# Kernel optimization log

Measured on AMD Instinct MI355X. Metric: run time of the kernel, lower is better.

## Reference

```python
import jax, jax.numpy as jnp
import numpy as np

TOP_K = 2


def setup_inputs() -> dict:
    key = jax.random.key(0)
    k1, k2, k3, k4 = jax.random.split(key, 4)
    B, S, D, F, E = 4, 2048, 1024, 4096, 8
    return {
        "inputs": jax.random.normal(k1, (B, S, D), dtype=jnp.float32),
        "gate_w": jax.random.normal(k2, (D, E), dtype=jnp.float32) * 0.02,
        "w1": jax.random.normal(k3, (E, D, F), dtype=jnp.float32) * 0.02,
        "w2": jax.random.normal(k4, (E, F, D), dtype=jnp.float32) * 0.02,
    }


def reference(inputs, gate_w, w1, w2):
    # gate logits: [B, S, E]
    gate_logits = jnp.einsum("bsd,de->bse", inputs, gate_w)
    E = gate_logits.shape[-1]

    # router KL loss (matches F.kl_div(log(mean_prob), uniform, reduction='batchmean')):
    # kl = sum(u * (log u - log p_mean)) / E   (batchmean divides by first dim = E)
    gate_prob = jax.nn.softmax(gate_logits.astype(jnp.float32), axis=-1).astype(inputs.dtype)
    mean_prob = gate_prob.mean(axis=(0, 1))  # [E]
    u = jnp.full((E,), 1.0 / E, dtype=mean_prob.dtype)
    kl_loss = jnp.sum(u * (jnp.log(u) - jnp.log(mean_prob))) / E

    # top-k routing
    weights, selected = jax.lax.top_k(gate_logits, TOP_K)  # [B,S,k]
    prob = jax.nn.softmax(weights.astype(jnp.float32), axis=-1).astype(inputs.dtype)

    # combine weight per expert: [B,S,E]; zero for unselected experts
    onehot = jax.nn.one_hot(selected, E, dtype=prob.dtype)  # [B,S,k,E]
    combine = jnp.einsum("bsk,bske->bse", prob, onehot)

    results = jnp.zeros_like(inputs)
    for i in range(E):  # fixed small loop over experts
        h = jax.nn.silu(jnp.einsum("bsd,df->bsf", inputs, w1[i]))
        out = jnp.einsum("bsf,fd->bsd", h, w2[i])
        results = results + combine[..., i : i + 1] * out
    return (results, kl_loss)
```

## Files before the change

### kernel.cpp

```cpp
#include <hip/hip_runtime.h>
#include <hip/hip_bf16.h>
#include <cstdint>


#define N_TOK 8192
#define D_DIM 1024
#define F_DIM 4096
#define N_EXP 8
#define MB_MAX 136

#define CNT_OFF   0u
#define HOFF_OFF  64u
#define NMB_OFF   104u
#define ZPG_OFF   128u
#define MBE_OFF   256u
#define MBB_OFF   896u
#define PSUM_OFF  1536u
#define LIST_OFF  67072u
#define COEF_OFF  329216u
#define H1_OFF    1048576ull
#define XBF_OFF   1048576ull
#define W1T_OFF   18874368ull
#define W2T_OFF   (W1T_OFF + 67108864ull)
#define H2_OFF    (W2T_OFF + 67108864ull)
#define FULL_WS   (H2_OFF + 17408ull * 4096ull * 2ull)

typedef __attribute__((ext_vector_type(8))) short short8;
typedef __attribute__((ext_vector_type(4))) float f32x4;
typedef __attribute__((ext_vector_type(4))) float float4v;
typedef __attribute__((ext_vector_type(2))) unsigned int u32x2;

__device__ __forceinline__ unsigned short f2bf(float x) {
  unsigned int u = __float_as_uint(x);
  unsigned int r = (u + 0x7fffu + ((u >> 16) & 1u)) >> 16;
  return (unsigned short)r;
}

__device__ __forceinline__ void gload16(const void* g, void* l) {
  __builtin_amdgcn_global_load_lds(
      (const __attribute__((address_space(1))) void*)g,
      (__attribute__((address_space(3))) void*)l, 16, 0, 0);
}

__global__ void router_kernel(const float* __restrict__ x,
                              const float* __restrict__ gw,
                              int* __restrict__ cnt, int* __restrict__ list,
                              float* __restrict__ coef,
                              float* __restrict__ psum,
                              unsigned short* __restrict__ xbf) {
  const int wave = threadIdx.x >> 6;
  const int lane = threadIdx.x & 63;
  const int t = blockIdx.x * 4 + wave;

  __shared__ float bps[N_EXP];
  if (threadIdx.x < N_EXP) bps[threadIdx.x] = 0.f;
  __syncthreads();

  float lg[8] = {0.f, 0.f, 0.f, 0.f, 0.f, 0.f, 0.f, 0.f};
  const float* xr = x + (size_t)t * D_DIM;
  unsigned short* xbr = xbf + (size_t)t * D_DIM;
#pragma unroll
  for (int i = 0; i < 16; ++i) {
    int d = lane + i * 64;
    float xv = xr[d];
    xbr[d] = f2bf(xv);
    float4v w0 = *(const float4v*)(gw + d * 8);
    float4v w1 = *(const float4v*)(gw + d * 8 + 4);
    lg[0] = fmaf(xv, w0.x, lg[0]); lg[1] = fmaf(xv, w0.y, lg[1]);
    lg[2] = fmaf(xv, w0.z, lg[2]); lg[3] = fmaf(xv, w0.w, lg[3]);
    lg[4] = fmaf(xv, w1.x, lg[4]); lg[5] = fmaf(xv, w1.y, lg[5]);
    lg[6] = fmaf(xv, w1.z, lg[6]); lg[7] = fmaf(xv, w1.w, lg[7]);
  }
#pragma unroll
  for (int m = 32; m; m >>= 1) {
#pragma unroll
    for (int e = 0; e < 8; ++e) lg[e] += __shfl_xor(lg[e], m);
  }

  if (lane == 0) {
    float mx = lg[0];
#pragma unroll
    for (int e = 1; e < 8; ++e) mx = fmaxf(mx, lg[e]);
    float p[8], s = 0.f;
#pragma unroll
    for (int e = 0; e < 8; ++e) { p[e] = expf(lg[e] - mx); s += p[e]; }
    float inv = 1.f / s;
#pragma unroll
    for (int e = 0; e < 8; ++e) atomicAdd(&bps[e], p[e] * inv);

    int i0 = 0;
#pragma unroll
    for (int e = 1; e < 8; ++e) if (lg[e] > lg[i0]) i0 = e;
    int i1 = (i0 == 0) ? 1 : 0;
#pragma unroll
    for (int e = 0; e < 8; ++e) if (e != i1 && e != i0 && lg[e] > lg[i1]) i1 = e;
    float p0 = 1.f / (1.f + expf(lg[i1] - lg[i0]));
    float p1 = 1.f - p0;
    int s0 = atomicAdd(&cnt[i0], 1);
    list[i0 * N_TOK + s0] = t; coef[i0 * N_TOK + s0] = p0;
    int s1 = atomicAdd(&cnt[i1], 1);
    list[i1 * N_TOK + s1] = t; coef[i1 * N_TOK + s1] = p1;
  }
  __syncthreads();
  if (threadIdx.x < 8) psum[blockIdx.x * 8 + threadIdx.x] = bps[threadIdx.x];
}

__global__ void prefix_kernel(const int* __restrict__ cnt, int* __restrict__ hoff,
                              int* __restrict__ mbe, int* __restrict__ mbb,
                              int* __restrict__ nmb, int g) {
  if (threadIdx.x == 0) {
    int o = 0, gmb = 0;
    for (int e = 0; e < 8; ++e) {
      hoff[e] = o;
      int nb = (cnt[e] + g - 1) / g;
      for (int m = 0; m < nb; ++m) { mbe[gmb] = e; mbb[gmb] = m; ++gmb; }
      o += nb * g;
    }
    hoff[8] = o;
    *nmb = gmb;
  }
}

__global__ void kl_kernel(const float* __restrict__ psum, float* __restrict__ out_kl) {
  __shared__ float s[8];
  if (threadIdx.x < 8) s[threadIdx.x] = 0.f;
  __syncthreads();
  float loc[8] = {0.f, 0.f, 0.f, 0.f, 0.f, 0.f, 0.f, 0.f};
  for (int r = threadIdx.x; r < 2048; r += 256) {
#pragma unroll
    for (int e = 0; e < 8; ++e) loc[e] += psum[r * 8 + e];
  }
#pragma unroll
  for (int e = 0; e < 8; ++e) atomicAdd(&s[e], loc[e]);
  __syncthreads();
  if (threadIdx.x == 0) {
    float kl = 0.f;
#pragma unroll
    for (int e = 0; e < 8; ++e) {
      float mean = s[e] / 8192.f;
      kl += (logf(0.125f) - logf(mean));
    }
    out_kl[0] = kl * (0.125f * 0.125f);
  }
}

__global__ __launch_bounds__(256) void wtrans_kernel(
    const float* __restrict__ w, unsigned short* __restrict__ wt, int K, int N) {
  const int e = blockIdx.z;
  const int n0 = blockIdx.x * 64, k0 = blockIdx.y * 64;
  __shared__ float t[64][65];
  const float* we = w + (size_t)e * K * N;
  const int nl = threadIdx.x & 63;
  const int kl4 = threadIdx.x >> 6;
#pragma unroll
  for (int r = 0; r < 16; ++r) {
    int kl = r * 4 + kl4;
    t[kl][nl] = we[(size_t)(k0 + kl) * N + n0 + nl];
  }
  __syncthreads();
  unsigned short* wte = wt + (size_t)e * K * N;
  const int kp = (threadIdx.x & 31) * 2;
  const int nl8 = threadIdx.x >> 5;
#pragma unroll
  for (int r = 0; r < 8; ++r) {
    int n = r * 8 + nl8;
    unsigned int pk = (unsigned int)f2bf(t[kp][n]) |
                      ((unsigned int)f2bf(t[kp + 1][n]) << 16);
    *(unsigned int*)(wte + (size_t)(n0 + n) * K + k0 + kp) = pk;
  }
}

__device__ __forceinline__ short8 ld_frag(const unsigned short* base, int row_base,
                                          int k_base, int lane) {
  int row = row_base + (lane & 15);
  int byte = (row * 128 + (k_base + ((lane >> 4) << 3)) * 2) ^ ((row & 7) << 4);
  return *(const short8*)((const char*)base + byte);
}

#define STAGE4(buf)                                                        \
  {                                                                        \
    char* la_ = (char*)As + (buf) * 16384 + wave * 1024;                   \
    char* lb_ = (char*)Bs + (buf) * 16384 + wave * 1024;                   \
    _Pragma("unroll") for (int i_ = 0; i_ < 4; ++i_) {                     \
      gload16(asrc[i_], la_ + i_ * 4096);                                  \
      gload16(bsrc[i_], lb_ + i_ * 4096);                                  \
      asrc[i_] += astep[i_];                                               \
      bsrc[i_] += 128;                                                     \
    }                                                                      \
  }

__global__ __launch_bounds__(256, 2) void gemm1_v4(
    const unsigned short* __restrict__ xbf, const unsigned short* __restrict__ w1t,
    const int* __restrict__ cnt, const int* __restrict__ hoff,
    const int* __restrict__ mbe, const int* __restrict__ mbb,
    const int* __restrict__ nmb,
    const int* __restrict__ list, const unsigned short* __restrict__ zpage,
    unsigned short* __restrict__ h) {
  const int mb = blockIdx.y;
  if (mb >= *nmb) return;
  const int e = mbe[mb], mblk = mbb[mb], nblk = blockIdx.x;
  const int c = cnt[e];
  const int tid = threadIdx.x, lane = tid & 63, wave = tid >> 6;
  const int wm = (wave >> 1) * 64, wn = (wave & 1) * 64;

  __shared__ unsigned short As[2][8192];
  __shared__ unsigned short Bs[2][8192];

  const int rowb = tid >> 3;
  const int sw = (((tid & 7) ^ (rowb & 7)) << 4);
  const char* asrc[4]; int astep[4];
  const char* bsrc[4];
#pragma unroll
  for (int i = 0; i < 4; ++i) {
    int row = i * 32 + rowb;
    int slot = mblk * 128 + row;
    if (slot < c) {
      int tok = list[e * N_TOK + slot];
      asrc[i] = (const char*)(xbf + (size_t)tok * D_DIM) + sw;
      astep[i] = 128;
    } else {
      asrc[i] = (const char*)zpage + sw;
      astep[i] = 0;
    }
    bsrc[i] = (const char*)(w1t + ((size_t)e * F_DIM + nblk * 128 + row) * D_DIM) + sw;
  }

  f32x4 acc[4][4];
#pragma unroll
  for (int i = 0; i < 4; ++i)
#pragma unroll
    for (int j = 0; j < 4; ++j) acc[i][j] = f32x4{0.f, 0.f, 0.f, 0.f};

  STAGE4(0);
  __syncthreads();
  int cur = 0;
  for (int kc = 0; kc < 16; ++kc) {
    if (kc + 1 < 16) STAGE4(cur ^ 1);
    const unsigned short* At = As[cur];
    const unsigned short* Bt = Bs[cur];
#pragma unroll
    for (int ks = 0; ks < 2; ++ks) {
      short8 af[4], bb[4];
#pragma unroll
      for (int mf = 0; mf < 4; ++mf) af[mf] = ld_frag(At, wm + mf * 16, ks * 32, lane);
#pragma unroll
      for (int nf = 0; nf < 4; ++nf) bb[nf] = ld_frag(Bt, wn + nf * 16, ks * 32, lane);
#pragma unroll
      for (int mf = 0; mf < 4; ++mf)
#pragma unroll
        for (int nf = 0; nf < 4; ++nf)
          acc[mf][nf] = __builtin_amdgcn_mfma_f32_16x16x32_bf16(
              af[mf], bb[nf], acc[mf][nf], 0, 0, 0);
    }
    __syncthreads();
    cur ^= 1;
  }

  const int hbase = hoff[e] + mblk * 128;
#pragma unroll
  for (int mf = 0; mf < 4; ++mf)
#pragma unroll
    for (int nf = 0; nf < 4; ++nf)
#pragma unroll
      for (int r = 0; r < 4; ++r) {
        float v = acc[mf][nf][r];
        v = v / (1.f + __expf(-v));
        int row = wm + mf * 16 + ((lane >> 4) << 2) + r;
        int col = nblk * 128 + wn + nf * 16 + (lane & 15);
        h[(size_t)(hbase + row) * F_DIM + col] = f2bf(v);
      }
}

__global__ __launch_bounds__(256, 2) void gemm2_v4(
    const unsigned short* __restrict__ h, const unsigned short* __restrict__ w2t,
    const int* __restrict__ cnt, const int* __restrict__ hoff,
    const int* __restrict__ mbe, const int* __restrict__ mbb,
    const int* __restrict__ nmb,
    const int* __restrict__ list, const float* __restrict__ coef,
    float* __restrict__ out) {
  const int mb = blockIdx.y;
  if (mb >= *nmb) return;
  const int e = mbe[mb], mblk = mbb[mb], nblk = blockIdx.x;
  const int c = cnt[e];
  const int tid = threadIdx.x, lane = tid & 63, wave = tid >> 6;
  const int wm = (wave >> 1) * 64, wn = (wave & 1) * 64;

  __shared__ unsigned short As[2][8192];
  __shared__ unsigned short Bs[2][8192];

  const int rowb = tid >> 3;
  const int sw = (((tid & 7) ^ (rowb & 7)) << 4);
  const int hbase = hoff[e] + mblk * 128;
  const char* asrc[4]; int astep[4];
  const char* bsrc[4];
#pragma unroll
  for (int i = 0; i < 4; ++i) {
    int row = i * 32 + rowb;
    asrc[i] = (const char*)(h + (size_t)(hbase + row) * F_DIM) + sw;
    astep[i] = 128;
    bsrc[i] = (const char*)(w2t + ((size_t)e * D_DIM + nblk * 128 + row) * F_DIM) + sw;
  }

  f32x4 acc[4][4];
#pragma unroll
  for (int i = 0; i < 4; ++i)
#pragma unroll
    for (int j = 0; j < 4; ++j) acc[i][j] = f32x4{0.f, 0.f, 0.f, 0.f};

  STAGE4(0);
  __syncthreads();
  int cur = 0;
  for (int kc = 0; kc < 64; ++kc) {
    if (kc + 1 < 64) STAGE4(cur ^ 1);
    const unsigned short* At = As[cur];
    const unsigned short* Bt = Bs[cur];
#pragma unroll
    for (int ks = 0; ks < 2; ++ks) {
      short8 af[4], bb[4];
#pragma unroll
      for (int mf = 0; mf < 4; ++mf) af[mf] = ld_frag(At, wm + mf * 16, ks * 32, lane);
#pragma unroll
      for (int nf = 0; nf < 4; ++nf) bb[nf] = ld_frag(Bt, wn + nf * 16, ks * 32, lane);
#pragma unroll
      for (int mf = 0; mf < 4; ++mf)
#pragma unroll
        for (int nf = 0; nf < 4; ++nf)
          acc[mf][nf] = __builtin_amdgcn_mfma_f32_16x16x32_bf16(
              af[mf], bb[nf], acc[mf][nf], 0, 0, 0);
    }
    __syncthreads();
    cur ^= 1;
  }

#pragma unroll
  for (int mf = 0; mf < 4; ++mf) {
#pragma unroll
    for (int r = 0; r < 4; ++r) {
      int slot = mblk * 128 + wm + mf * 16 + ((lane >> 4) << 2) + r;
      if (slot < c) {
        int tok = list[e * N_TOK + slot];
        float cf = coef[e * N_TOK + slot];
#pragma unroll
        for (int nf = 0; nf < 4; ++nf) {
          int col = nblk * 128 + wn + nf * 16 + (lane & 15);
          unsafeAtomicAdd(&out[(size_t)tok * D_DIM + col], cf * acc[mf][nf][r]);
        }
      }
    }
  }
}

__global__ __launch_bounds__(256) void gemm1_v1(
    const float* __restrict__ x, const float* __restrict__ w1,
    const int* __restrict__ cnt, const int* __restrict__ hoff,
    const int* __restrict__ list, unsigned short* __restrict__ h) {
  const int e = blockIdx.z, mblk = blockIdx.y, nblk = blockIdx.x;
  const int c = cnt[e];
  if (mblk * 128 >= c) return;
  const int tid = threadIdx.x, lane = tid & 63, wave = tid >> 6;
  const int wm = (wave >> 1) * 64, wn = (wave & 1) * 64;

  __shared__ unsigned short At[128 * 64];
  __shared__ unsigned short Bt[128 * 64];
  __shared__ int toks[128];
  if (tid < 128) {
    int slot = mblk * 128 + tid;
    toks[tid] = (slot < c) ? list[e * N_TOK + slot] : -1;
  }
  __syncthreads();

  f32x4 acc[4][4];
#pragma unroll
  for (int i = 0; i < 4; ++i)
#pragma unroll
    for (int j = 0; j < 4; ++j) acc[i][j] = f32x4{0.f, 0.f, 0.f, 0.f};

  const float* w1e = w1 + (size_t)e * D_DIM * F_DIM;
  for (int kc = 0; kc < 16; ++kc) {
    __syncthreads();
#pragma unroll
    for (int it = 0; it < 8; ++it) {
      int lin = it * 256 + tid;
      int row = lin >> 4, c4 = lin & 15;
      int tok = toks[row];
      unsigned int lo = 0u, hi = 0u;
      if (tok >= 0) {
        float4v f = *(const float4v*)(x + (size_t)tok * D_DIM + kc * 64 + c4 * 4);
        lo = (unsigned int)f2bf(f.x) | ((unsigned int)f2bf(f.y) << 16);
        hi = (unsigned int)f2bf(f.z) | ((unsigned int)f2bf(f.w) << 16);
      }
      int byte = (row * 128 + c4 * 8) ^ ((row & 7) << 4);
      *(u32x2*)((char*)At + byte) = u32x2{lo, hi};
    }
#pragma unroll
    for (int it = 0; it < 16; ++it) {
      int lin = it * 256 + tid;
      int f_loc = lin & 127, dp = lin >> 7;
      int d = kc * 64 + dp * 2;
      const float* src = w1e + (size_t)d * F_DIM + nblk * 128 + f_loc;
      unsigned int pk = (unsigned int)f2bf(src[0]) |
                        ((unsigned int)f2bf(src[F_DIM]) << 16);
      int byte = (f_loc * 128 + dp * 4) ^ ((f_loc & 7) << 4);
      *(unsigned int*)((char*)Bt + byte) = pk;
    }
    __syncthreads();
#pragma unroll
    for (int ks = 0; ks < 2; ++ks) {
      short8 af[4], bb[4];
#pragma unroll
      for (int mf = 0; mf < 4; ++mf) af[mf] = ld_frag(At, wm + mf * 16, ks * 32, lane);
#pragma unroll
      for (int nf = 0; nf < 4; ++nf) bb[nf] = ld_frag(Bt, wn + nf * 16, ks * 32, lane);
#pragma unroll
      for (int mf = 0; mf < 4; ++mf)
#pragma unroll
        for (int nf = 0; nf < 4; ++nf)
          acc[mf][nf] = __builtin_amdgcn_mfma_f32_16x16x32_bf16(
              af[mf], bb[nf], acc[mf][nf], 0, 0, 0);
    }
  }

  const int hbase = hoff[e] + mblk * 128;
#pragma unroll
  for (int mf = 0; mf < 4; ++mf)
#pragma unroll
    for (int nf = 0; nf < 4; ++nf)
#pragma unroll
      for (int r = 0; r < 4; ++r) {
        float v = acc[mf][nf][r];
        v = v / (1.f + __expf(-v));
        int row = wm + mf * 16 + ((lane >> 4) << 2) + r;
        int col = nblk * 128 + wn + nf * 16 + (lane & 15);
        h[(size_t)(hbase + row) * F_DIM + col] = f2bf(v);
      }
}

__global__ __launch_bounds__(256) void gemm2_v1(
    const unsigned short* __restrict__ h, const float* __restrict__ w2,
    const int* __restrict__ cnt, const int* __restrict__ hoff,
    const int* __restrict__ list, const float* __restrict__ coef,
    float* __restrict__ out) {
  const int e = blockIdx.z, mblk = blockIdx.y, nblk = blockIdx.x;
  const int c = cnt[e];
  if (mblk * 128 >= c) return;
  const int tid = threadIdx.x, lane = tid & 63, wave = tid >> 6;
  const int wm = (wave >> 1) * 64, wn = (wave & 1) * 64;

  __shared__ unsigned short At[128 * 64];
  __shared__ unsigned short Bt[128 * 64];

  f32x4 acc[4][4];
#pragma unroll
  for (int i = 0; i < 4; ++i)
#pragma unroll
    for (int j = 0; j < 4; ++j) acc[i][j] = f32x4{0.f, 0.f, 0.f, 0.f};

  const int hbase = hoff[e] + mblk * 128;
  const float* w2e = w2 + (size_t)e * F_DIM * D_DIM;
  for (int kc = 0; kc < 64; ++kc) {
    __syncthreads();
#pragma unroll
    for (int it = 0; it < 8; ++it) {
      int lin = it * 256 + tid;
      int row = lin >> 4, c4 = lin & 15;
      u32x2 v = *(const u32x2*)(h + (size_t)(hbase + row) * F_DIM + kc * 64 + c4 * 4);
      int byte = (row * 128 + c4 * 8) ^ ((row & 7) << 4);
      *(u32x2*)((char*)At + byte) = v;
    }
#pragma unroll
    for (int it = 0; it < 16; ++it) {
      int lin = it * 256 + tid;
      int dcol = lin & 127, kp = lin >> 7;
      int k = kc * 64 + kp * 2;
      const float* src = w2e + (size_t)k * D_DIM + nblk * 128 + dcol;
      unsigned int pk = (unsigned int)f2bf(src[0]) |
                        ((unsigned int)f2bf(src[D_DIM]) << 16);
      int byte = (dcol * 128 + kp * 4) ^ ((dcol & 7) << 4);
      *(unsigned int*)((char*)Bt + byte) = pk;
    }
    __syncthreads();
#pragma unroll
    for (int ks = 0; ks < 2; ++ks) {
      short8 af[4], bb[4];
#pragma unroll
      for (int mf = 0; mf < 4; ++mf) af[mf] = ld_frag(At, wm + mf * 16, ks * 32, lane);
#pragma unroll
      for (int nf = 0; nf < 4; ++nf) bb[nf] = ld_frag(Bt, wn + nf * 16, ks * 32, lane);
#pragma unroll
      for (int mf = 0; mf < 4; ++mf)
#pragma unroll
        for (int nf = 0; nf < 4; ++nf)
          acc[mf][nf] = __builtin_amdgcn_mfma_f32_16x16x32_bf16(
              af[mf], bb[nf], acc[mf][nf], 0, 0, 0);
    }
  }

#pragma unroll
  for (int mf = 0; mf < 4; ++mf) {
#pragma unroll
    for (int r = 0; r < 4; ++r) {
      int slot = mblk * 128 + wm + mf * 16 + ((lane >> 4) << 2) + r;
      if (slot < c) {
        int tok = list[e * N_TOK + slot];
        float cf = coef[e * N_TOK + slot];
#pragma unroll
        for (int nf = 0; nf < 4; ++nf) {
          int col = nblk * 128 + wn + nf * 16 + (lane & 15);
          unsafeAtomicAdd(&out[(size_t)tok * D_DIM + col], cf * acc[mf][nf][r]);
        }
      }
    }
  }
}

extern "C" void kernel_launch(void* const* d_in, const int* in_sizes, int n_in,
                              void* d_out, int out_size, void* d_ws, size_t ws_size,
                              hipStream_t stream) {
  const float* x = (const float*)d_in[0];
  const float* gw = (const float*)d_in[1];
  const float* w1 = (const float*)d_in[2];
  const float* w2 = (const float*)d_in[3];
  float* out = (float*)d_out;
  char* ws = (char*)d_ws;

  int* cnt = (int*)(ws + CNT_OFF);
  int* hoff = (int*)(ws + HOFF_OFF);
  int* nmb = (int*)(ws + NMB_OFF);
  int* mbe = (int*)(ws + MBE_OFF);
  int* mbb = (int*)(ws + MBB_OFF);
  float* psum = (float*)(ws + PSUM_OFF);
  int* list = (int*)(ws + LIST_OFF);
  float* coef = (float*)(ws + COEF_OFF);
  unsigned short* xbf = (unsigned short*)(ws + XBF_OFF);

  hipMemsetAsync(d_ws, 0, PSUM_OFF + 2048 * 8 * 4, stream);
  hipMemsetAsync(d_out, 0, (size_t)out_size * 4, stream);

  router_kernel<<<2048, 256, 0, stream>>>(x, gw, cnt, list, coef, psum, xbf);
  prefix_kernel<<<1, 64, 0, stream>>>(cnt, hoff, mbe, mbb, nmb, 128);
  kl_kernel<<<1, 256, 0, stream>>>(psum, out + 8388608);

  if (ws_size >= FULL_WS) {
    unsigned short* w1t = (unsigned short*)(ws + W1T_OFF);
    unsigned short* w2t = (unsigned short*)(ws + W2T_OFF);
    unsigned short* h = (unsigned short*)(ws + H2_OFF);
    const unsigned short* zpage = (const unsigned short*)(ws + ZPG_OFF);

    wtrans_kernel<<<dim3(64, 16, 8), 256, 0, stream>>>(w1, w1t, 1024, 4096);
    wtrans_kernel<<<dim3(16, 64, 8), 256, 0, stream>>>(w2, w2t, 4096, 1024);
    gemm1_v4<<<dim3(32, MB_MAX), 256, 0, stream>>>(xbf, w1t, cnt, hoff, mbe, mbb,
                                                   nmb, list, zpage, h);
    gemm2_v4<<<dim3(8, MB_MAX), 256, 0, stream>>>(h, w2t, cnt, hoff, mbe, mbb,
                                                  nmb, list, coef, out);
  } else {
    unsigned short* h = (unsigned short*)(ws + H1_OFF);
    gemm1_v1<<<dim3(32, 64, 8), 256, 0, stream>>>(x, w1, cnt, hoff, list, h);
    gemm2_v1<<<dim3(8, 64, 8), 256, 0, stream>>>(h, w2, cnt, hoff, list, coef, out);
  }
}
```

Baseline: 956.7 us.

## Enlarge grouped GEMM tiles to 256x256 with 8 waves and split-K gemm2

Both expert GEMMs move from 128x128 tiles with 4 waves to 256x256 tiles with 8 waves, each wave holding a 128x64 accumulator. This raises arithmetic intensity and cuts redundant global loads of the weights and activations. The K loop now uses explicit vmcnt waits, fenced barriers and s_setprio around the MFMA bursts to overlap loads with compute. gemm2 also splits K across two z-blocks that combine through the existing atomic adds. The costs are heavier register and LDS pressure, more padding waste per expert at the 256-row granularity, and extra atomic traffic.

```diff
diff --git a/kernel.cpp b/kernel.cpp
--- a/kernel.cpp
+++ b/kernel.cpp
@@ -7,7 +7,7 @@
 #define D_DIM 1024
 #define F_DIM 4096
 #define N_EXP 8
-#define MB_MAX 136
+#define MB_MAX 72
 
 #define CNT_OFF   0u
 #define HOFF_OFF  64u
@@ -23,7 +23,7 @@
 #define W1T_OFF   18874368ull
 #define W2T_OFF   (W1T_OFF + 67108864ull)
 #define H2_OFF    (W2T_OFF + 67108864ull)
-#define FULL_WS   (H2_OFF + 17408ull * 4096ull * 2ull)
+#define FULL_WS   (H2_OFF + 18432ull * 4096ull * 2ull)
 
 typedef __attribute__((ext_vector_type(8))) short short8;
 typedef __attribute__((ext_vector_type(4))) float f32x4;
@@ -177,19 +177,56 @@
   return *(const short8*)((const char*)base + byte);
 }
 
-#define STAGE4(buf)                                                        \
+#define ISSUE(b)                                                           \
   {                                                                        \
-    char* la_ = (char*)As + (buf) * 16384 + wave * 1024;                   \
-    char* lb_ = (char*)Bs + (buf) * 16384 + wave * 1024;                   \
+    char* la_ = (char*)&As[b][0] + tid * 16;                               \
+    char* lb_ = (char*)&Bs[b][0] + tid * 16;                               \
     _Pragma("unroll") for (int i_ = 0; i_ < 4; ++i_) {                     \
-      gload16(asrc[i_], la_ + i_ * 4096);                                  \
-      gload16(bsrc[i_], lb_ + i_ * 4096);                                  \
+      gload16(asrc[i_], la_ + i_ * 8192);                                  \
+      gload16(bsrc[i_], lb_ + i_ * 8192);                                  \
       asrc[i_] += astep[i_];                                               \
       bsrc[i_] += 128;                                                     \
     }                                                                      \
   }
 
-__global__ __launch_bounds__(256, 2) void gemm1_v4(
+#define COMPUTE(b)                                                         \
+  _Pragma("unroll") for (int ks_ = 0; ks_ < 2; ++ks_) {                    \
+    short8 af[8], bb[4];                                                   \
+    _Pragma("unroll") for (int mf_ = 0; mf_ < 8; ++mf_)                    \
+      af[mf_] = ld_frag(&As[b][0], wm + mf_ * 16, ks_ * 32, lane);         \
+    _Pragma("unroll") for (int nf_ = 0; nf_ < 4; ++nf_)                    \
+      bb[nf_] = ld_frag(&Bs[b][0], wn + nf_ * 16, ks_ * 32, lane);         \
+    __builtin_amdgcn_s_setprio(1);                                         \
+    _Pragma("unroll") for (int mf_ = 0; mf_ < 8; ++mf_)                    \
+      _Pragma("unroll") for (int nf_ = 0; nf_ < 4; ++nf_)                  \
+        acc[mf_][nf_] = __builtin_amdgcn_mfma_f32_16x16x32_bf16(           \
+            af[mf_], bb[nf_], acc[mf_][nf_], 0, 0, 0);                     \
+    __builtin_amdgcn_s_setprio(0);                                         \
+  }
+
+#define BAR_FENCED()                                                       \
+  __builtin_amdgcn_sched_barrier(0);                                       \
+  __builtin_amdgcn_s_barrier();                                            \
+  __builtin_amdgcn_sched_barrier(0);
+
+#define KLOOP(NT)                                                          \
+  ISSUE(0);                                                                \
+  {                                                                        \
+    int cur = 0;                                                           \
+    for (int t_ = 0; t_ < (NT) - 1; ++t_) {                                \
+      ISSUE(cur ^ 1);                                                      \
+      asm volatile("s_waitcnt vmcnt(8)" ::: "memory");                     \
+      BAR_FENCED();                                                        \
+      if (cur) { COMPUTE(1); } else { COMPUTE(0); }                        \
+      BAR_FENCED();                                                        \
+      cur ^= 1;                                                            \
+    }                                                                      \
+    asm volatile("s_waitcnt vmcnt(0)" ::: "memory");                       \
+    BAR_FENCED();                                                          \
+    if (cur) { COMPUTE(1); } else { COMPUTE(0); }                          \
+  }
+
+__global__ __launch_bounds__(512, 2) void gemm1_v5(
     const unsigned short* __restrict__ xbf, const unsigned short* __restrict__ w1t,
     const int* __restrict__ cnt, const int* __restrict__ hoff,
     const int* __restrict__ mbe, const int* __restrict__ mbb,
@@ -201,10 +238,10 @@
   const int e = mbe[mb], mblk = mbb[mb], nblk = blockIdx.x;
   const int c = cnt[e];
   const int tid = threadIdx.x, lane = tid & 63, wave = tid >> 6;
-  const int wm = (wave >> 1) * 64, wn = (wave & 1) * 64;
-
-  __shared__ unsigned short As[2][8192];
-  __shared__ unsigned short Bs[2][8192];
+  const int wm = (wave >> 2) * 128, wn = (wave & 3) * 64;
+
+  __shared__ unsigned short As[2][16384];
+  __shared__ unsigned short Bs[2][16384];
 
   const int rowb = tid >> 3;
   const int sw = (((tid & 7) ^ (rowb & 7)) << 4);
@@ -212,8 +249,8 @@
   const char* bsrc[4];
 #pragma unroll
   for (int i = 0; i < 4; ++i) {
-    int row = i * 32 + rowb;
-    int slot = mblk * 128 + row;
+    int row = i * 64 + rowb;
+    int slot = mblk * 256 + row;
     if (slot < c) {
       int tok = list[e * N_TOK + slot];
       asrc[i] = (const char*)(xbf + (size_t)tok * D_DIM) + sw;
@@ -222,43 +259,20 @@
       asrc[i] = (const char*)zpage + sw;
       astep[i] = 0;
     }
-    bsrc[i] = (const char*)(w1t + ((size_t)e * F_DIM + nblk * 128 + row) * D_DIM) + sw;
-  }
-
-  f32x4 acc[4][4];
-#pragma unroll
-  for (int i = 0; i < 4; ++i)
+    bsrc[i] = (const char*)(w1t + ((size_t)e * F_DIM + nblk * 256 + row) * D_DIM) + sw;
+  }
+
+  f32x4 acc[8][4];
+#pragma unroll
+  for (int i = 0; i < 8; ++i)
 #pragma unroll
     for (int j = 0; j < 4; ++j) acc[i][j] = f32x4{0.f, 0.f, 0.f, 0.f};
 
-  STAGE4(0);
-  __syncthreads();
-  int cur = 0;
-  for (int kc = 0; kc < 16; ++kc) {
-    if (kc + 1 < 16) STAGE4(cur ^ 1);
-    const unsigned short* At = As[cur];
-    const unsigned short* Bt = Bs[cur];
-#pragma unroll
-    for (int ks = 0; ks < 2; ++ks) {
-      short8 af[4], bb[4];
-#pragma unroll
-      for (int mf = 0; mf < 4; ++mf) af[mf] = ld_frag(At, wm + mf * 16, ks * 32, lane);
-#pragma unroll
-      for (int nf = 0; nf < 4; ++nf) bb[nf] = ld_frag(Bt, wn + nf * 16, ks * 32, lane);
-#pragma unroll
-      for (int mf = 0; mf < 4; ++mf)
-#pragma unroll
-        for (int nf = 0; nf < 4; ++nf)
-          acc[mf][nf] = __builtin_amdgcn_mfma_f32_16x16x32_bf16(
-              af[mf], bb[nf], acc[mf][nf], 0, 0, 0);
-    }
-    __syncthreads();
-    cur ^= 1;
-  }
-
-  const int hbase = hoff[e] + mblk * 128;
-#pragma unroll
-  for (int mf = 0; mf < 4; ++mf)
+  KLOOP(16);
+
+  const int hbase = hoff[e] + mblk * 256;
+#pragma unroll
+  for (int mf = 0; mf < 8; ++mf)
 #pragma unroll
     for (int nf = 0; nf < 4; ++nf)
 #pragma unroll
@@ -266,12 +280,12 @@
         float v = acc[mf][nf][r];
         v = v / (1.f + __expf(-v));
         int row = wm + mf * 16 + ((lane >> 4) << 2) + r;
-        int col = nblk * 128 + wn + nf * 16 + (lane & 15);
+        int col = nblk * 256 + wn + nf * 16 + (lane & 15);
         h[(size_t)(hbase + row) * F_DIM + col] = f2bf(v);
       }
 }
 
-__global__ __launch_bounds__(256, 2) void gemm2_v4(
+__global__ __launch_bounds__(512, 2) void gemm2_v5(
     const unsigned short* __restrict__ h, const unsigned short* __restrict__ w2t,
     const int* __restrict__ cnt, const int* __restrict__ hoff,
     const int* __restrict__ mbe, const int* __restrict__ mbb,
@@ -282,67 +296,45 @@
   if (mb >= *nmb) return;
   const int e = mbe[mb], mblk = mbb[mb], nblk = blockIdx.x;
   const int c = cnt[e];
+  const int kofs = blockIdx.z * 2048;
   const int tid = threadIdx.x, lane = tid & 63, wave = tid >> 6;
-  const int wm = (wave >> 1) * 64, wn = (wave & 1) * 64;
-
-  __shared__ unsigned short As[2][8192];
-  __shared__ unsigned short Bs[2][8192];
+  const int wm = (wave >> 2) * 128, wn = (wave & 3) * 64;
+
+  __shared__ unsigned short As[2][16384];
+  __shared__ unsigned short Bs[2][16384];
 
   const int rowb = tid >> 3;
   const int sw = (((tid & 7) ^ (rowb & 7)) << 4);
-  const int hbase = hoff[e] + mblk * 128;
+  const int hbase = hoff[e] + mblk * 256;
   const char* asrc[4]; int astep[4];
   const char* bsrc[4];
 #pragma unroll
   for (int i = 0; i < 4; ++i) {
-    int row = i * 32 + rowb;
-    asrc[i] = (const char*)(h + (size_t)(hbase + row) * F_DIM) + sw;
+    int row = i * 64 + rowb;
+    asrc[i] = (const char*)(h + (size_t)(hbase + row) * F_DIM + kofs) + sw;
     astep[i] = 128;
-    bsrc[i] = (const char*)(w2t + ((size_t)e * D_DIM + nblk * 128 + row) * F_DIM) + sw;
-  }
-
-  f32x4 acc[4][4];
-#pragma unroll
-  for (int i = 0; i < 4; ++i)
+    bsrc[i] = (const char*)(w2t + ((size_t)e * D_DIM + nblk * 256 + row) * F_DIM + kofs) + sw;
+  }
+
+  f32x4 acc[8][4];
+#pragma unroll
+  for (int i = 0; i < 8; ++i)
 #pragma unroll
     for (int j = 0; j < 4; ++j) acc[i][j] = f32x4{0.f, 0.f, 0.f, 0.f};
 
-  STAGE4(0);
-  __syncthreads();
-  int cur = 0;
-  for (int kc = 0; kc < 64; ++kc) {
-    if (kc + 1 < 64) STAGE4(cur ^ 1);
-    const unsigned short* At = As[cur];
-    const unsigned short* Bt = Bs[cur];
-#pragma unroll
-    for (int ks = 0; ks < 2; ++ks) {
-      short8 af[4], bb[4];
-#pragma unroll
-      for (int mf = 0; mf < 4; ++mf) af[mf] = ld_frag(At, wm + mf * 16, ks * 32, lane);
-#pragma unroll
-      for (int nf = 0; nf < 4; ++nf) bb[nf] = ld_frag(Bt, wn + nf * 16, ks * 32, lane);
-#pragma unroll
-      for (int mf = 0; mf < 4; ++mf)
-#pragma unroll
-        for (int nf = 0; nf < 4; ++nf)
-          acc[mf][nf] = __builtin_amdgcn_mfma_f32_16x16x32_bf16(
-              af[mf], bb[nf], acc[mf][nf], 0, 0, 0);
-    }
-    __syncthreads();
-    cur ^= 1;
-  }
-
-#pragma unroll
-  for (int mf = 0; mf < 4; ++mf) {
+  KLOOP(32);
+
+#pragma unroll
+  for (int mf = 0; mf < 8; ++mf) {
 #pragma unroll
     for (int r = 0; r < 4; ++r) {
-      int slot = mblk * 128 + wm + mf * 16 + ((lane >> 4) << 2) + r;
+      int slot = mblk * 256 + wm + mf * 16 + ((lane >> 4) << 2) + r;
       if (slot < c) {
         int tok = list[e * N_TOK + slot];
         float cf = coef[e * N_TOK + slot];
 #pragma unroll
         for (int nf = 0; nf < 4; ++nf) {
-          int col = nblk * 128 + wn + nf * 16 + (lane & 15);
+          int col = nblk * 256 + wn + nf * 16 + (lane & 15);
           unsafeAtomicAdd(&out[(size_t)tok * D_DIM + col], cf * acc[mf][nf][r]);
         }
       }
@@ -533,14 +525,16 @@
   float* coef = (float*)(ws + COEF_OFF);
   unsigned short* xbf = (unsigned short*)(ws + XBF_OFF);
 
+  const bool full = (ws_size >= FULL_WS);
+
   hipMemsetAsync(d_ws, 0, PSUM_OFF + 2048 * 8 * 4, stream);
   hipMemsetAsync(d_out, 0, (size_t)out_size * 4, stream);
 
   router_kernel<<<2048, 256, 0, stream>>>(x, gw, cnt, list, coef, psum, xbf);
-  prefix_kernel<<<1, 64, 0, stream>>>(cnt, hoff, mbe, mbb, nmb, 128);
+  prefix_kernel<<<1, 64, 0, stream>>>(cnt, hoff, mbe, mbb, nmb, full ? 256 : 128);
   kl_kernel<<<1, 256, 0, stream>>>(psum, out + 8388608);
 
-  if (ws_size >= FULL_WS) {
+  if (full) {
     unsigned short* w1t = (unsigned short*)(ws + W1T_OFF);
     unsigned short* w2t = (unsigned short*)(ws + W2T_OFF);
     unsigned short* h = (unsigned short*)(ws + H2_OFF);
@@ -548,10 +542,10 @@
 
     wtrans_kernel<<<dim3(64, 16, 8), 256, 0, stream>>>(w1, w1t, 1024, 4096);
     wtrans_kernel<<<dim3(16, 64, 8), 256, 0, stream>>>(w2, w2t, 4096, 1024);
-    gemm1_v4<<<dim3(32, MB_MAX), 256, 0, stream>>>(xbf, w1t, cnt, hoff, mbe, mbb,
+    gemm1_v5<<<dim3(16, MB_MAX), 512, 0, stream>>>(xbf, w1t, cnt, hoff, mbe, mbb,
                                                    nmb, list, zpage, h);
-    gemm2_v4<<<dim3(8, MB_MAX), 256, 0, stream>>>(h, w2t, cnt, hoff, mbe, mbb,
-                                                  nmb, list, coef, out);
+    gemm2_v5<<<dim3(4, MB_MAX, 2), 512, 0, stream>>>(h, w2t, cnt, hoff, mbe, mbb,
+                                                     nmb, list, coef, out);
   } else {
     unsigned short* h = (unsigned short*)(ws + H1_OFF);
     gemm1_v1<<<dim3(32, 64, 8), 256, 0, stream>>>(x, w1, cnt, hoff, list, h);
```

New measurement: 2.941 ms. 3.07x slower.

## Enlarge expert GEMM M-tile to 256 rows with 512 threads and split-K GEMM2

Applied to the files above, without the earlier changes.

Both expert GEMMs now use 256-row token tiles computed by 8 waves (512 threads), so each weight tile loaded into shared memory is reused across twice as many tokens. The second GEMM also splits its K dimension (F) in two along a new grid axis; the halves combine through the existing atomic adds into the output. The routing prefix kernel now pads expert segments to 256 rows, and the workspace size for the hidden buffer grows to match. In exchange, the explicit LDS double buffering is replaced by a single buffer with a barrier before and after each load, which gives up intra-block overlap of loads and MFMA work and relies on the extra waves for latency hiding.

```diff
diff --git a/kernel.cpp b/kernel.cpp
--- a/kernel.cpp
+++ b/kernel.cpp
@@ -7,7 +7,7 @@
 #define D_DIM 1024
 #define F_DIM 4096
 #define N_EXP 8
-#define MB_MAX 136
+#define MB_MAX 72
 
 #define CNT_OFF   0u
 #define HOFF_OFF  64u
@@ -23,7 +23,7 @@
 #define W1T_OFF   18874368ull
 #define W2T_OFF   (W1T_OFF + 67108864ull)
 #define H2_OFF    (W2T_OFF + 67108864ull)
-#define FULL_WS   (H2_OFF + 17408ull * 4096ull * 2ull)
+#define FULL_WS   (H2_OFF + 18432ull * 4096ull * 2ull)
 
 typedef __attribute__((ext_vector_type(8))) short short8;
 typedef __attribute__((ext_vector_type(4))) float f32x4;
@@ -177,19 +177,7 @@
   return *(const short8*)((const char*)base + byte);
 }
 
-#define STAGE4(buf)                                                        \
-  {                                                                        \
-    char* la_ = (char*)As + (buf) * 16384 + wave * 1024;                   \
-    char* lb_ = (char*)Bs + (buf) * 16384 + wave * 1024;                   \
-    _Pragma("unroll") for (int i_ = 0; i_ < 4; ++i_) {                     \
-      gload16(asrc[i_], la_ + i_ * 4096);                                  \
-      gload16(bsrc[i_], lb_ + i_ * 4096);                                  \
-      asrc[i_] += astep[i_];                                               \
-      bsrc[i_] += 128;                                                     \
-    }                                                                      \
-  }
-
-__global__ __launch_bounds__(256, 2) void gemm1_v4(
+__global__ __launch_bounds__(512, 2) void gemm1_v6(
     const unsigned short* __restrict__ xbf, const unsigned short* __restrict__ w1t,
     const int* __restrict__ cnt, const int* __restrict__ hoff,
     const int* __restrict__ mbe, const int* __restrict__ mbb,
@@ -203,17 +191,17 @@
   const int tid = threadIdx.x, lane = tid & 63, wave = tid >> 6;
   const int wm = (wave >> 1) * 64, wn = (wave & 1) * 64;
 
-  __shared__ unsigned short As[2][8192];
-  __shared__ unsigned short Bs[2][8192];
+  __shared__ unsigned short As[256 * 64];
+  __shared__ unsigned short Bs[128 * 64];
 
   const int rowb = tid >> 3;
   const int sw = (((tid & 7) ^ (rowb & 7)) << 4);
   const char* asrc[4]; int astep[4];
-  const char* bsrc[4];
+  const char* bsrc[2];
 #pragma unroll
   for (int i = 0; i < 4; ++i) {
-    int row = i * 32 + rowb;
-    int slot = mblk * 128 + row;
+    int row = i * 64 + rowb;
+    int slot = mblk * 256 + row;
     if (slot < c) {
       int tok = list[e * N_TOK + slot];
       asrc[i] = (const char*)(xbf + (size_t)tok * D_DIM) + sw;
@@ -222,6 +210,10 @@
       asrc[i] = (const char*)zpage + sw;
       astep[i] = 0;
     }
+  }
+#pragma unroll
+  for (int i = 0; i < 2; ++i) {
+    int row = i * 64 + rowb;
     bsrc[i] = (const char*)(w1t + ((size_t)e * F_DIM + nblk * 128 + row) * D_DIM) + sw;
   }
 
@@ -231,20 +223,26 @@
 #pragma unroll
     for (int j = 0; j < 4; ++j) acc[i][j] = f32x4{0.f, 0.f, 0.f, 0.f};
 
-  STAGE4(0);
-  __syncthreads();
-  int cur = 0;
   for (int kc = 0; kc < 16; ++kc) {
-    if (kc + 1 < 16) STAGE4(cur ^ 1);
-    const unsigned short* At = As[cur];
-    const unsigned short* Bt = Bs[cur];
+    __syncthreads();
+#pragma unroll
+    for (int i = 0; i < 4; ++i) {
+      gload16(asrc[i], (char*)As + i * 8192 + tid * 16);
+      asrc[i] += astep[i];
+    }
+#pragma unroll
+    for (int i = 0; i < 2; ++i) {
+      gload16(bsrc[i], (char*)Bs + i * 8192 + tid * 16);
+      bsrc[i] += 128;
+    }
+    __syncthreads();
 #pragma unroll
     for (int ks = 0; ks < 2; ++ks) {
       short8 af[4], bb[4];
 #pragma unroll
-      for (int mf = 0; mf < 4; ++mf) af[mf] = ld_frag(At, wm + mf * 16, ks * 32, lane);
-#pragma unroll
-      for (int nf = 0; nf < 4; ++nf) bb[nf] = ld_frag(Bt, wn + nf * 16, ks * 32, lane);
+      for (int mf = 0; mf < 4; ++mf) af[mf] = ld_frag(As, wm + mf * 16, ks * 32, lane);
+#pragma unroll
+      for (int nf = 0; nf < 4; ++nf) bb[nf] = ld_frag(Bs, wn + nf * 16, ks * 32, lane);
 #pragma unroll
       for (int mf = 0; mf < 4; ++mf)
 #pragma unroll
@@ -252,11 +250,9 @@
           acc[mf][nf] = __builtin_amdgcn_mfma_f32_16x16x32_bf16(
               af[mf], bb[nf], acc[mf][nf], 0, 0, 0);
     }
-    __syncthreads();
-    cur ^= 1;
-  }
-
-  const int hbase = hoff[e] + mblk * 128;
+  }
+
+  const int hbase = hoff[e] + mblk * 256;
 #pragma unroll
   for (int mf = 0; mf < 4; ++mf)
 #pragma unroll
@@ -271,7 +267,7 @@
       }
 }
 
-__global__ __launch_bounds__(256, 2) void gemm2_v4(
+__global__ __launch_bounds__(512, 2) void gemm2_v6(
     const unsigned short* __restrict__ h, const unsigned short* __restrict__ w2t,
     const int* __restrict__ cnt, const int* __restrict__ hoff,
     const int* __restrict__ mbe, const int* __restrict__ mbb,
@@ -282,23 +278,27 @@
   if (mb >= *nmb) return;
   const int e = mbe[mb], mblk = mbb[mb], nblk = blockIdx.x;
   const int c = cnt[e];
+  const int kofs = blockIdx.z * 2048;
   const int tid = threadIdx.x, lane = tid & 63, wave = tid >> 6;
   const int wm = (wave >> 1) * 64, wn = (wave & 1) * 64;
 
-  __shared__ unsigned short As[2][8192];
-  __shared__ unsigned short Bs[2][8192];
+  __shared__ unsigned short As[256 * 64];
+  __shared__ unsigned short Bs[128 * 64];
 
   const int rowb = tid >> 3;
   const int sw = (((tid & 7) ^ (rowb & 7)) << 4);
-  const int hbase = hoff[e] + mblk * 128;
-  const char* asrc[4]; int astep[4];
-  const char* bsrc[4];
+  const int hbase = hoff[e] + mblk * 256;
+  const char* asrc[4];
+  const char* bsrc[2];
 #pragma unroll
   for (int i = 0; i < 4; ++i) {
-    int row = i * 32 + rowb;
-    asrc[i] = (const char*)(h + (size_t)(hbase + row) * F_DIM) + sw;
-    astep[i] = 128;
-    bsrc[i] = (const char*)(w2t + ((size_t)e * D_DIM + nblk * 128 + row) * F_DIM) + sw;
+    int row = i * 64 + rowb;
+    asrc[i] = (const char*)(h + (size_t)(hbase + row) * F_DIM + kofs) + sw;
+  }
+#pragma unroll
+  for (int i = 0; i < 2; ++i) {
+    int row = i * 64 + rowb;
+    bsrc[i] = (const char*)(w2t + ((size_t)e * D_DIM + nblk * 128 + row) * F_DIM + kofs) + sw;
   }
 
   f32x4 acc[4][4];
@@ -307,20 +307,26 @@
 #pragma unroll
     for (int j = 0; j < 4; ++j) acc[i][j] = f32x4{0.f, 0.f, 0.f, 0.f};
 
-  STAGE4(0);
-  __syncthreads();
-  int cur = 0;
-  for (int kc = 0; kc < 64; ++kc) {
-    if (kc + 1 < 64) STAGE4(cur ^ 1);
-    const unsigned short* At = As[cur];
-    const unsigned short* Bt = Bs[cur];
+  for (int kc = 0; kc < 32; ++kc) {
+    __syncthreads();
+#pragma unroll
+    for (int i = 0; i < 4; ++i) {
+      gload16(asrc[i], (char*)As + i * 8192 + tid * 16);
+      asrc[i] += 128;
+    }
+#pragma unroll
+    for (int i = 0; i < 2; ++i) {
+      gload16(bsrc[i], (char*)Bs + i * 8192 + tid * 16);
+      bsrc[i] += 128;
+    }
+    __syncthreads();
 #pragma unroll
     for (int ks = 0; ks < 2; ++ks) {
       short8 af[4], bb[4];
 #pragma unroll
-      for (int mf = 0; mf < 4; ++mf) af[mf] = ld_frag(At, wm + mf * 16, ks * 32, lane);
-#pragma unroll
-      for (int nf = 0; nf < 4; ++nf) bb[nf] = ld_frag(Bt, wn + nf * 16, ks * 32, lane);
+      for (int mf = 0; mf < 4; ++mf) af[mf] = ld_frag(As, wm + mf * 16, ks * 32, lane);
+#pragma unroll
+      for (int nf = 0; nf < 4; ++nf) bb[nf] = ld_frag(Bs, wn + nf * 16, ks * 32, lane);
 #pragma unroll
       for (int mf = 0; mf < 4; ++mf)
 #pragma unroll
@@ -328,15 +334,13 @@
           acc[mf][nf] = __builtin_amdgcn_mfma_f32_16x16x32_bf16(
               af[mf], bb[nf], acc[mf][nf], 0, 0, 0);
     }
-    __syncthreads();
-    cur ^= 1;
   }
 
 #pragma unroll
   for (int mf = 0; mf < 4; ++mf) {
 #pragma unroll
     for (int r = 0; r < 4; ++r) {
-      int slot = mblk * 128 + wm + mf * 16 + ((lane >> 4) << 2) + r;
+      int slot = mblk * 256 + wm + mf * 16 + ((lane >> 4) << 2) + r;
       if (slot < c) {
         int tok = list[e * N_TOK + slot];
         float cf = coef[e * N_TOK + slot];
@@ -533,14 +537,16 @@
   float* coef = (float*)(ws + COEF_OFF);
   unsigned short* xbf = (unsigned short*)(ws + XBF_OFF);
 
+  const bool full = (ws_size >= FULL_WS);
+
   hipMemsetAsync(d_ws, 0, PSUM_OFF + 2048 * 8 * 4, stream);
   hipMemsetAsync(d_out, 0, (size_t)out_size * 4, stream);
 
   router_kernel<<<2048, 256, 0, stream>>>(x, gw, cnt, list, coef, psum, xbf);
-  prefix_kernel<<<1, 64, 0, stream>>>(cnt, hoff, mbe, mbb, nmb, 128);
+  prefix_kernel<<<1, 64, 0, stream>>>(cnt, hoff, mbe, mbb, nmb, full ? 256 : 128);
   kl_kernel<<<1, 256, 0, stream>>>(psum, out + 8388608);
 
-  if (ws_size >= FULL_WS) {
+  if (full) {
     unsigned short* w1t = (unsigned short*)(ws + W1T_OFF);
     unsigned short* w2t = (unsigned short*)(ws + W2T_OFF);
     unsigned short* h = (unsigned short*)(ws + H2_OFF);
@@ -548,10 +554,10 @@
 
     wtrans_kernel<<<dim3(64, 16, 8), 256, 0, stream>>>(w1, w1t, 1024, 4096);
     wtrans_kernel<<<dim3(16, 64, 8), 256, 0, stream>>>(w2, w2t, 4096, 1024);
-    gemm1_v4<<<dim3(32, MB_MAX), 256, 0, stream>>>(xbf, w1t, cnt, hoff, mbe, mbb,
+    gemm1_v6<<<dim3(32, MB_MAX), 512, 0, stream>>>(xbf, w1t, cnt, hoff, mbe, mbb,
                                                    nmb, list, zpage, h);
-    gemm2_v4<<<dim3(8, MB_MAX), 256, 0, stream>>>(h, w2t, cnt, hoff, mbe, mbb,
-                                                  nmb, list, coef, out);
+    gemm2_v6<<<dim3(8, MB_MAX, 2), 512, 0, stream>>>(h, w2t, cnt, hoff, mbe, mbb,
+                                                     nmb, list, coef, out);
   } else {
     unsigned short* h = (unsigned short*)(ws + H1_OFF);
     gemm1_v1<<<dim3(32, 64, 8), 256, 0, stream>>>(x, w1, cnt, hoff, list, h);
```

After: 878.3 us. 1.09x faster.
